# Optimization experiments

Measured on AMD Instinct MI355X. Metric: run time of the kernel, lower is better.

Reference implementation:

```python
import jax, jax.numpy as jnp
import numpy as np

# Fano-plane triples defining octonion multiplication: e_a e_b = e_c (cyclic)
_TRIPLES = [(1, 2, 4), (2, 3, 5), (3, 4, 6), (4, 5, 7), (5, 6, 1), (6, 7, 2), (7, 1, 3)]


def _oct_structure():
    """S3[i,j,k] = sign s.t. e_i * e_j = s * e_k (zero otherwise)."""
    idx = np.zeros((8, 8), dtype=np.int32)
    sgn = np.zeros((8, 8), dtype=np.float32)
    for j in range(8):
        idx[0, j] = j; sgn[0, j] = 1.0
    for i in range(1, 8):
        idx[i, 0] = i; sgn[i, 0] = 1.0
        idx[i, i] = 0; sgn[i, i] = -1.0
    for a, b, c in _TRIPLES:
        for (p, q, r) in ((a, b, c), (b, c, a), (c, a, b)):
            idx[p, q] = r; sgn[p, q] = 1.0
            idx[q, p] = r; sgn[q, p] = -1.0
    S3 = np.zeros((8, 8, 8), dtype=np.float32)
    for i in range(8):
        for j in range(8):
            S3[i, j, idx[i, j]] = sgn[i, j]
    return jnp.asarray(S3)


def _oct_full(W, S3):
    """Fold octonion structure into a dense block matrix.

    W: [8, out8, in8] per-component weights. Effective map:
      y_k = sum_{i,j} S3[i,j,k] * W_i @ x_j  ->  M[k*out8:, j*in8:] = sum_i S3[i,j,k] W_i
    Returns [8*out8, 8*in8].
    """
    M = jnp.einsum('ijk,ion->kojn', S3, W)  # [8, out8, 8, in8]
    k8, o8, j8, n8 = M.shape
    return M.reshape(k8 * o8, j8 * n8)


def setup_inputs() -> dict:
    key = jax.random.key(0)
    ks = jax.random.split(key, 6)
    B, T, D = 8, 1024, 1024
    S = 2048  # d_state = n_embd * expand_factor
    x = jax.random.normal(ks[0], (B, T, D), dtype=jnp.float32)
    h_prev = jnp.zeros((B, S), dtype=jnp.float32)
    WA = jax.random.normal(ks[1], (8, S // 8, S // 8), dtype=jnp.float32) * float(1.0 / np.sqrt(S))
    WB = jax.random.normal(ks[2], (8, S // 8, D // 8), dtype=jnp.float32) * float(1.0 / np.sqrt(D))
    WC = jax.random.normal(ks[3], (8, D // 8, S // 8), dtype=jnp.float32) * float(1.0 / np.sqrt(S))
    Wdelta = jax.random.normal(ks[4], (S, D), dtype=jnp.float32) * float(1.0 / np.sqrt(D))
    delta_bias = jnp.full((S,), -2.0, dtype=jnp.float32)
    return dict(x=x, h_prev=h_prev, WA=WA, WB=WB, WC=WC, Wdelta=Wdelta, delta_bias=delta_bias)


def reference(x, h_prev, WA, WB, WC, Wdelta, delta_bias):
    S3 = _oct_structure()
    Af = _oct_full(WA, S3)  # [S, S]
    Bf = _oct_full(WB, S3)  # [S, D]
    Cf = _oct_full(WC, S3)  # [D, S]
    # Selective gate: sigmoid(x @ Wdelta^T + bias)  [B, T, S]
    delta = jax.nn.sigmoid(jnp.einsum('btd,sd->bts', x, Wdelta) + delta_bias)
    # Input injection precomputed for all timesteps (B is time-invariant)
    Bx = jnp.einsum('btd,sd->bts', x, Bf)  # [B, T, S]

    def step(h, inp):
        bx_t, d_t = inp  # [B, S], [B, S]
        h_new = (1.0 - d_t) * h + d_t * (h @ Af.T + bx_t)
        return h_new, h_new

    h_last, hs = jax.lax.scan(step, h_prev, (jnp.swapaxes(Bx, 0, 1), jnp.swapaxes(delta, 0, 1)))
    # Readout applied to the full state history at once: y[t] = C(h[t])
    y = jnp.einsum('tbs,ds->btd', hs, Cf)  # [B, T, D]
    return y, h_last
```

## Files before the change

### kernel.cpp

```cpp
#include <hip/hip_runtime.h>
#include <hip/hip_bf16.h>

#define T_STEPS 1024
#define OFF_AFT   0ull
#define OFF_GCAT  4194304ull
#define OFF_CFT   8388608ull
#define OFF_DELTA 10485760ull
#define OFF_BX    27262976ull
#define OFF_HS    44040192ull
#define OFF_HBUF  60817408ull
#define OFF_CNT   60850176ull

typedef short short8 __attribute__((ext_vector_type(8)));
typedef float f32x4 __attribute__((ext_vector_type(4)));

__device__ __forceinline__ void build_oct_tables(int tid, int (*Is)[8], float (*Sg)[8]) {
  if (tid < 64) {
    int i = tid >> 3, j = tid & 7;
    int k = 0; float s = 0.f;
    if (i == 0)      { k = j; s = 1.f; }
    else if (j == 0) { k = i; s = 1.f; }
    else if (i == j) { k = 0; s = -1.f; }
    else {
      const int T7[7][3] = {{1,2,4},{2,3,5},{3,4,6},{4,5,7},{5,6,1},{6,7,2},{7,1,3}};
      for (int t = 0; t < 7; ++t) {
        int a = T7[t][0], b = T7[t][1], c = T7[t][2];
        const int P[3][3] = {{a,b,c},{b,c,a},{c,a,b}};
        for (int r = 0; r < 3; ++r) {
          if (i == P[r][0] && j == P[r][1]) { k = P[r][2]; s = 1.f; }
          if (i == P[r][1] && j == P[r][0]) { k = P[r][2]; s = -1.f; }
        }
      }
    }
    Is[j][k] = i; Sg[j][k] = s;
  }
  __syncthreads();
}

__device__ __forceinline__ unsigned short bf16r(float x) {
  unsigned u = __float_as_uint(x);
  return (unsigned short)((u + 0x7FFFu + ((u >> 16) & 1u)) >> 16);
}

__global__ __launch_bounds__(256) void fold_Ab(const float* __restrict__ WA, unsigned short* __restrict__ AfB) {
  __shared__ int Is[8][8]; __shared__ float Sg[8][8];
  build_oct_tables(threadIdx.x, Is, Sg);
  int g8 = blockIdx.x * 256 + threadIdx.x;
  int sp = g8 >> 8;
  int s0 = (g8 & 255) * 8;
  int k8 = sp >> 8, o = sp & 255;
  int j8 = s0 >> 8, n = s0 & 255;
  int i = Is[j8][k8]; float sg = Sg[j8][k8];
  const float* src = WA + (size_t)i * 65536 + (size_t)o * 256 + n;
  float4 f0 = *(const float4*)(src);
  float4 f1 = *(const float4*)(src + 4);
  unsigned short v[8];
  v[0] = bf16r(sg * f0.x); v[1] = bf16r(sg * f0.y); v[2] = bf16r(sg * f0.z); v[3] = bf16r(sg * f0.w);
  v[4] = bf16r(sg * f1.x); v[5] = bf16r(sg * f1.y); v[6] = bf16r(sg * f1.z); v[7] = bf16r(sg * f1.w);
  *(short8*)(AfB + (size_t)g8 * 8) = *(short8*)v;
}

__global__ __launch_bounds__(256) void fold_GC(const float* __restrict__ Wd, const float* __restrict__ WB,
                                               float* __restrict__ Gcat) {
  __shared__ int Is[8][8]; __shared__ float Sg[8][8];
  build_oct_tables(threadIdx.x, Is, Sg);
  int g4 = blockIdx.x * 256 + threadIdx.x;
  int col = (g4 & 1023) * 4;
  int d = g4 >> 10;
  float4 v;
  if (col < 2048) {
    v.x = Wd[(size_t)(col + 0) * 1024 + d];
    v.y = Wd[(size_t)(col + 1) * 1024 + d];
    v.z = Wd[(size_t)(col + 2) * 1024 + d];
    v.w = Wd[(size_t)(col + 3) * 1024 + d];
  } else {
    int sp = col - 2048;
    int k = sp >> 8;
    int j = d >> 7, n = d & 127;
    int i = Is[j][k]; float sg = Sg[j][k];
    const float* wb = WB + (size_t)i * 32768 + n;
    v.x = sg * wb[(size_t)((sp + 0) & 255) * 128];
    v.y = sg * wb[(size_t)((sp + 1) & 255) * 128];
    v.z = sg * wb[(size_t)((sp + 2) & 255) * 128];
    v.w = sg * wb[(size_t)((sp + 3) & 255) * 128];
  }
  *(float4*)(Gcat + (size_t)g4 * 4) = v;
}

__global__ __launch_bounds__(256) void fold_C(const float* __restrict__ WC, float* __restrict__ CfT) {
  __shared__ int Is[8][8]; __shared__ float Sg[8][8];
  build_oct_tables(threadIdx.x, Is, Sg);
  int g4 = blockIdx.x * 256 + threadIdx.x;
  int d0 = (g4 & 255) * 4;
  int s  = g4 >> 8;
  int j = s >> 8, n = s & 255;
  int k = d0 >> 7;
  int i = Is[j][k]; float sg = Sg[j][k];
  const float* wc = WC + (size_t)i * 32768 + n;
  float4 v;
  v.x = sg * wc[(size_t)((d0 + 0) & 127) * 256];
  v.y = sg * wc[(size_t)((d0 + 1) & 127) * 256];
  v.z = sg * wc[(size_t)((d0 + 2) & 127) * 256];
  v.w = sg * wc[(size_t)((d0 + 3) & 127) * 256];
  *(float4*)(CfT + (size_t)g4 * 4) = v;
}

__global__ __launch_bounds__(256) void init_h(const float* __restrict__ h_prev, unsigned long long* __restrict__ hx,
                                              int* __restrict__ cnt) {
  int gid = blockIdx.x * 256 + threadIdx.x;
  if (gid < 8192) {
    int c = gid >> 6, within = gid & 63;
    int pr = within >> 3, b = within & 7;
    int s = c * 16 + pr * 2;
    unsigned pk = (unsigned)bf16r(h_prev[(size_t)b * 2048 + s])
                | ((unsigned)bf16r(h_prev[(size_t)b * 2048 + s + 1]) << 16);
    hx[gid] = ((unsigned long long)pk << 32) | 0ull;
  } else {
    hx[gid] = 0x00000000FFFFFFFFull;
  }
  if (gid < 16) cnt[gid] = 0;
}

__global__ __launch_bounds__(512) void scan_dbx(const unsigned short* __restrict__ AfB,
                                                float* __restrict__ dlt, float* __restrict__ Bx,
                                                float* __restrict__ hs,
                                                unsigned long long* __restrict__ hx,
                                                const float* __restrict__ h_prev, float* __restrict__ hlast,
                                                const float* __restrict__ X, const float* __restrict__ G,
                                                const float* __restrict__ bias, int* __restrict__ chunkCnt) {
  __shared__ __attribute__((aligned(16))) unsigned short Sm[4 * 128 * 40];
  const int bid = blockIdx.x;
  const int tid = threadIdx.x;
  const int lane = tid & 63;

  if (bid >= 128) {
    const int gi = bid - 128;
    const int bn = gi & 31;
    const int bmSeq = gi >> 5;
    const int ck = bmSeq >> 3, bb = bmSeq & 7;
    const int bm = ck + 8 * bb;
    unsigned short* Ah = Sm;
    unsigned short* Al = Ah + 128 * 40;
    unsigned short* Bh = Al + 128 * 40;
    unsigned short* Bl = Bh + 128 * 40;
    const int w8 = tid >> 6;
    const int wr = w8 >> 2, wc = w8 & 3;
    const int lr = lane & 15, lk = lane >> 4;

    f32x4 acc[4][2];
    #pragma unroll
    for (int a = 0; a < 4; ++a) { acc[a][0] = (f32x4){0.f,0.f,0.f,0.f}; acc[a][1] = (f32x4){0.f,0.f,0.f,0.f}; }

    for (int kt = 0; kt < 1024; kt += 32) {
      {
        int row = tid >> 2, kq = tid & 3;
        const float* ar = X + (size_t)(bm * 128 + row) * 1024 + kt + kq * 8;
        float4 f0 = *(const float4*)(ar);
        float4 f1 = *(const float4*)(ar + 4);
        float vv[8] = {f0.x, f0.y, f0.z, f0.w, f1.x, f1.y, f1.z, f1.w};
        unsigned* ah32 = (unsigned*)Ah + row * 20 + kq * 4;
        unsigned* al32 = (unsigned*)Al + row * 20 + kq * 4;
        #pragma unroll
        for (int j = 0; j < 4; ++j) {
          unsigned short h0 = bf16r(vv[2 * j]), h1 = bf16r(vv[2 * j + 1]);
          float r0 = vv[2 * j]     - __uint_as_float((unsigned)h0 << 16);
          float r1 = vv[2 * j + 1] - __uint_as_float((unsigned)h1 << 16);
          ah32[j] = (unsigned)h0 | ((unsigned)h1 << 16);
          al32[j] = (unsigned)bf16r(r0) | ((unsigned)bf16r(r1) << 16);
        }
      }
      {
        int kr = tid >> 4, cg = tid & 15;
        const float* br = G + (size_t)(kt + kr) * 4096 + bn * 128 + cg * 8;
        float4 f0 = *(const float4*)(br);
        float4 f1 = *(const float4*)(br + 4);
        float vv[8] = {f0.x, f0.y, f0.z, f0.w, f1.x, f1.y, f1.z, f1.w};
        #pragma unroll
        for (int e = 0; e < 8; ++e) {
          int n = cg * 8 + e;
          unsigned short h = bf16r(vv[e]);
          float r = vv[e] - __uint_as_float((unsigned)h << 16);
          Bh[n * 40 + kr] = h;
          Bl[n * 40 + kr] = bf16r(r);
        }
      }
      __syncthreads();
      short8 ahf[4], alf[4], bhf[2], blf[2];
      #pragma unroll
      for (int f = 0; f < 4; ++f) {
        int ma = (wr * 64 + f * 16 + lr) * 40 + lk * 8;
        ahf[f] = *(const short8*)(Ah + ma);
        alf[f] = *(const short8*)(Al + ma);
      }
      #pragma unroll
      for (int e = 0; e < 2; ++e) {
        int nb2 = (wc * 32 + e * 16 + lr) * 40 + lk * 8;
        bhf[e] = *(const short8*)(Bh + nb2);
        blf[e] = *(const short8*)(Bl + nb2);
      }
      #pragma unroll
      for (int fm = 0; fm < 4; ++fm)
        #pragma unroll
        for (int fn = 0; fn < 2; ++fn) {
          acc[fm][fn] = __builtin_amdgcn_mfma_f32_16x16x32_bf16(ahf[fm], bhf[fn], acc[fm][fn], 0, 0, 0);
          acc[fm][fn] = __builtin_amdgcn_mfma_f32_16x16x32_bf16(ahf[fm], blf[fn], acc[fm][fn], 0, 0, 0);
          acc[fm][fn] = __builtin_amdgcn_mfma_f32_16x16x32_bf16(alf[fm], bhf[fn], acc[fm][fn], 0, 0, 0);
        }
      __syncthreads();
    }
    const bool isDelta = (bn < 16);
    #pragma unroll
    for (int fm = 0; fm < 4; ++fm) {
      #pragma unroll
      for (int rr = 0; rr < 4; ++rr) {
        int r = bm * 128 + wr * 64 + fm * 16 + lk * 4 + rr;
        int t = r & 1023, b = r >> 10;
        size_t base = ((size_t)t * 8 + b) * 2048;
        #pragma unroll
        for (int fn = 0; fn < 2; ++fn) {
          int n = bn * 128 + wc * 32 + fn * 16 + lr;
          float v = acc[fm][fn][rr];
          if (isDelta) {
            v += bias[n];
            v = 1.0f / (1.0f + expf(-v));
            __hip_atomic_store(&dlt[base + n], v, __ATOMIC_RELAXED, __HIP_MEMORY_SCOPE_SYSTEM);
          } else {
            __hip_atomic_store(&Bx[base + (n - 2048)], v, __ATOMIC_RELAXED, __HIP_MEMORY_SCOPE_SYSTEM);
          }
        }
      }
    }
    __syncthreads();
    if (tid == 0)
      __hip_atomic_fetch_add(&chunkCnt[ck], 1, __ATOMIC_RELAXED, __HIP_MEMORY_SCOPE_SYSTEM);
    return;
  }

  float* red = (float*)Sm;
  const int wg = bid;
  const int w = tid >> 6;
  const int row = lane & 15;
  const int g4 = lane >> 4;
  const int nb = lane & 7;

  short8 afr[8];
  {
    const unsigned short* ab = AfB + (size_t)(wg * 16 + row) * 2048 + w * 256 + g4 * 8;
    #pragma unroll
    for (int q = 0; q < 8; ++q)
      afr[q] = *(const short8*)(ab + q * 32);
  }
  const int S0 = (g4 & 1) * 32 + nb;

  const int ub = tid >> 3, usp = (tid & 7) * 2;
  const int pword = wg * 64 + (tid & 7) * 8 + ub;
  float hr0 = 0.f, hr1 = 0.f;
  if (tid < 64) {
    hr0 = h_prev[(size_t)ub * 2048 + wg * 16 + usp];
    hr1 = h_prev[(size_t)ub * 2048 + wg * 16 + usp + 1];
  }

  #pragma unroll 1
  for (int t = 0; t < T_STEPS; ++t) {
    float2 dv = make_float2(0.f, 0.f), bxv = make_float2(0.f, 0.f);
    if (tid < 64) {
      if ((t & 127) == 0) {
        const int ck = t >> 7;
        while (__hip_atomic_load(&chunkCnt[ck], __ATOMIC_RELAXED, __HIP_MEMORY_SCOPE_SYSTEM) < 256)
          __builtin_amdgcn_s_sleep(16);
      }
      size_t off = ((size_t)t * 8 + ub) * 2048 + wg * 16 + usp;
      dv  = *(const float2*)(dlt + off);
      bxv = *(const float2*)(Bx + off);
    }
    const unsigned want = (unsigned)t;
    const unsigned long long* bq = hx + (size_t)(t & 1) * 8192 + (size_t)w * 1024 + lane;
    unsigned long long wv[16];
    #pragma unroll
    for (int p = 0; p < 16; ++p)
      wv[p] = __hip_atomic_load(bq + p * 64, __ATOMIC_RELAXED, __HIP_MEMORY_SCOPE_SYSTEM);
    int fails = 0;
    for (;;) {
      bool stale = false;
      #pragma unroll
      for (int p = 0; p < 16; ++p) stale |= ((unsigned)wv[p] != want);
      if (!__any(stale)) break;
      if (++fails > 4) __builtin_amdgcn_s_sleep(1);
      #pragma unroll
      for (int p = 0; p < 16; ++p)
        if ((unsigned)wv[p] != want)
          wv[p] = __hip_atomic_load(bq + p * 64, __ATOMIC_RELAXED, __HIP_MEMORY_SCOPE_SYSTEM);
    }
    unsigned hi[16];
    #pragma unroll
    for (int p = 0; p < 16; ++p) hi[p] = (unsigned)(wv[p] >> 32);

    f32x4 acc = {0.f, 0.f, 0.f, 0.f};
    #pragma unroll
    for (int q = 0; q < 8; ++q) {
      union { unsigned d[4]; short8 v; } bb;
      #pragma unroll
      for (int u = 0; u < 4; ++u) {
        int S = S0 + u * 8;
        unsigned c0 = __shfl(hi[2 * q],     S, 64);
        unsigned c1 = __shfl(hi[2 * q + 1], S, 64);
        bb.d[u] = (g4 & 2) ? c1 : c0;
      }
      acc = __builtin_amdgcn_mfma_f32_16x16x32_bf16(afr[q], bb.v, acc, 0, 0, 0);
    }
    if (row < 8) {
      #pragma unroll
      for (int r = 0; r < 4; ++r)
        red[w * 144 + (g4 * 4 + r) * 9 + row] = acc[r];
    }
    __syncthreads();
    if (tid < 64) {
      __builtin_amdgcn_s_setprio(1);
      float o0 = 0.f, o1 = 0.f;
      #pragma unroll
      for (int ww = 0; ww < 8; ++ww) {
        o0 += red[ww * 144 + usp * 9 + ub];
        o1 += red[ww * 144 + (usp + 1) * 9 + ub];
      }
      float h0 = fmaf(dv.x, o0 + bxv.x - hr0, hr0);
      float h1 = fmaf(dv.y, o1 + bxv.y - hr1, hr1);
      hr0 = h0; hr1 = h1;
      unsigned pk = (unsigned)bf16r(h0) | ((unsigned)bf16r(h1) << 16);
      unsigned long long wval = ((unsigned long long)pk << 32) | (unsigned long long)(unsigned)(t + 1);
      __hip_atomic_store(hx + (size_t)((t + 1) & 1) * 8192 + pword, wval,
                         __ATOMIC_RELAXED, __HIP_MEMORY_SCOPE_SYSTEM);
      __builtin_amdgcn_s_setprio(0);
      size_t off = ((size_t)t * 8 + ub) * 2048 + wg * 16 + usp;
      *(float2*)(hs + off) = make_float2(h0, h1);
      if (t == T_STEPS - 1)
        *(float2*)(hlast + (size_t)ub * 2048 + wg * 16 + usp) = make_float2(h0, h1);
    }
    __syncthreads();
  }
}

__global__ __launch_bounds__(256) void gemm_y(const float* __restrict__ HS, const float* __restrict__ CfT,
                                              float* __restrict__ out) {
  __shared__ unsigned short As[128 * 40];
  __shared__ unsigned short Bs[128 * 40];
  const int bn = blockIdx.x, bm = blockIdx.y;
  const int tid = threadIdx.x;
  const int lane = tid & 63;
  const int w = tid >> 6;
  const int wr = w >> 1, wc = w & 1;
  const int lr = lane & 15, lk = lane >> 4;

  f32x4 acc[4][4];
  #pragma unroll
  for (int a = 0; a < 4; ++a)
    #pragma unroll
    for (int b = 0; b < 4; ++b) acc[a][b] = (f32x4){0.f, 0.f, 0.f, 0.f};

  for (int kt = 0; kt < 2048; kt += 32) {
    {
      int row = tid >> 1, kh = tid & 1;
      int rg = bm * 128 + row;
      const float* ar = HS + (size_t)((rg & 1023) * 8 + (rg >> 10)) * 2048 + kt + kh * 16;
      float vv[16];
      #pragma unroll
      for (int q = 0; q < 4; ++q) {
        float4 f = *(const float4*)(ar + q * 4);
        vv[q * 4 + 0] = f.x; vv[q * 4 + 1] = f.y; vv[q * 4 + 2] = f.z; vv[q * 4 + 3] = f.w;
      }
      unsigned* a32 = (unsigned*)As + row * 20 + kh * 8;
      #pragma unroll
      for (int j = 0; j < 8; ++j)
        a32[j] = (unsigned)bf16r(vv[2 * j]) | ((unsigned)bf16r(vv[2 * j + 1]) << 16);
    }
    {
      int kr = tid >> 3, cg = tid & 7;
      const float* br = CfT + (size_t)(kt + kr) * 1024 + bn * 128 + cg * 16;
      #pragma unroll
      for (int q = 0; q < 4; ++q) {
        float4 f = *(const float4*)(br + q * 4);
        float vv[4] = {f.x, f.y, f.z, f.w};
        #pragma unroll
        for (int e = 0; e < 4; ++e)
          Bs[(cg * 16 + q * 4 + e) * 40 + kr] = bf16r(vv[e]);
      }
    }
    __syncthreads();
    short8 aF[4], bF[4];
    #pragma unroll
    for (int f = 0; f < 4; ++f) {
      aF[f] = *(const short8*)(As + (wr * 64 + f * 16 + lr) * 40 + lk * 8);
      bF[f] = *(const short8*)(Bs + (wc * 64 + f * 16 + lr) * 40 + lk * 8);
    }
    #pragma unroll
    for (int fm = 0; fm < 4; ++fm)
      #pragma unroll
      for (int fn = 0; fn < 4; ++fn)
        acc[fm][fn] = __builtin_amdgcn_mfma_f32_16x16x32_bf16(aF[fm], bF[fn], acc[fm][fn], 0, 0, 0);
    __syncthreads();
  }
  #pragma unroll
  for (int fm = 0; fm < 4; ++fm)
    #pragma unroll
    for (int rr = 0; rr < 4; ++rr) {
      size_t rg = bm * 128 + wr * 64 + fm * 16 + lk * 4 + rr;
      #pragma unroll
      for (int fn = 0; fn < 4; ++fn) {
        int n = bn * 128 + wc * 64 + fn * 16 + lr;
        out[rg * 1024 + n] = acc[fm][fn][rr];
      }
    }
}

extern "C" void kernel_launch(void* const* d_in, const int* in_sizes, int n_in,
                              void* d_out, int out_size, void* d_ws, size_t ws_size,
                              hipStream_t stream) {
  const float* x      = (const float*)d_in[0];
  const float* h_prev = (const float*)d_in[1];
  const float* WA     = (const float*)d_in[2];
  const float* WB     = (const float*)d_in[3];
  const float* WC     = (const float*)d_in[4];
  const float* Wd     = (const float*)d_in[5];
  const float* bias   = (const float*)d_in[6];
  float* out = (float*)d_out;
  float* w = (float*)d_ws;
  unsigned short* AfB = (unsigned short*)(w + OFF_AFT);
  float* Gcat = w + OFF_GCAT;
  float* CfT  = w + OFF_CFT;
  float* dlt  = w + OFF_DELTA;
  float* Bx   = w + OFF_BX;
  float* hs   = w + OFF_HS;
  unsigned long long* hx = (unsigned long long*)(w + OFF_HBUF);
  int* chunkCnt = (int*)(w + OFF_CNT);

  fold_Ab<<<2048, 256, 0, stream>>>(WA, AfB);
  fold_GC<<<4096, 256, 0, stream>>>(Wd, WB, Gcat);
  fold_C <<<2048, 256, 0, stream>>>(WC, CfT);
  init_h <<<64,   256, 0, stream>>>(h_prev, hx, chunkCnt);
  scan_dbx<<<2176, 512, 0, stream>>>(AfB, dlt, Bx, hs, hx, h_prev, out + 8388608,
                                     x, Gcat, bias, chunkCnt);
  gemm_y<<<dim3(8, 64), 256, 0, stream>>>(hs, CfT, out);
}
```

Baseline: 3.704 ms.

## Fuse readout GEMM into scan kernel, overlapping it with the recurrence per chunk

Drops the separate gemm_y launch and adds 512 extra blocks to the persistent scan kernel. Each new block waits on a per-128-timestep progress counter, then computes its 128x128 readout tile from the finished hidden states. This lets the readout run on otherwise idle CUs while the sequential scan continues. The scan now double-buffers its reduction scratch, writes hs with atomic stores and bumps the counter after a vmcnt wait. The risks are spin-waiting blocks taking CU slots the scan blocks need (a deadlock if the scheduler runs them first) and extra memory-ordering overhead in the latency-critical scan loop.

```diff
diff --git a/kernel.cpp b/kernel.cpp
--- a/kernel.cpp
+++ b/kernel.cpp
@@ -118,20 +118,95 @@
   } else {
     hx[gid] = 0x00000000FFFFFFFFull;
   }
-  if (gid < 16) cnt[gid] = 0;
-}
-
-__global__ __launch_bounds__(512) void scan_dbx(const unsigned short* __restrict__ AfB,
-                                                float* __restrict__ dlt, float* __restrict__ Bx,
-                                                float* __restrict__ hs,
-                                                unsigned long long* __restrict__ hx,
-                                                const float* __restrict__ h_prev, float* __restrict__ hlast,
-                                                const float* __restrict__ X, const float* __restrict__ G,
-                                                const float* __restrict__ bias, int* __restrict__ chunkCnt) {
+  if (gid < 32) cnt[gid] = 0;
+}
+
+__global__ __launch_bounds__(512) void scan_dbx_y(const unsigned short* __restrict__ AfB,
+                                                  float* __restrict__ dlt, float* __restrict__ Bx,
+                                                  float* __restrict__ hs,
+                                                  unsigned long long* __restrict__ hx,
+                                                  const float* __restrict__ h_prev, float* __restrict__ hlast,
+                                                  const float* __restrict__ X, const float* __restrict__ G,
+                                                  const float* __restrict__ bias,
+                                                  const float* __restrict__ CfT, float* __restrict__ out,
+                                                  int* __restrict__ chunkCnt, int* __restrict__ scanProg) {
   __shared__ __attribute__((aligned(16))) unsigned short Sm[4 * 128 * 40];
   const int bid = blockIdx.x;
   const int tid = threadIdx.x;
   const int lane = tid & 63;
+
+  if (bid >= 2176) {
+    const int gi = bid - 2176;
+    const int ck = gi >> 6;
+    const int idx = gi & 63;
+    const int bm = (idx >> 3) * 8 + ck;
+    const int bn = idx & 7;
+    if (tid == 0) {
+      while (__hip_atomic_load(&scanProg[ck], __ATOMIC_RELAXED, __HIP_MEMORY_SCOPE_SYSTEM) < 128)
+        __builtin_amdgcn_s_sleep(32);
+    }
+    __syncthreads();
+    unsigned short* As = Sm;
+    unsigned short* Bs = Sm + 128 * 40;
+    const int w8 = tid >> 6;
+    const int wr = w8 >> 2, wc = w8 & 3;
+    const int lr = lane & 15, lk = lane >> 4;
+
+    f32x4 acc[4][2];
+    #pragma unroll
+    for (int a = 0; a < 4; ++a) { acc[a][0] = (f32x4){0.f,0.f,0.f,0.f}; acc[a][1] = (f32x4){0.f,0.f,0.f,0.f}; }
+
+    for (int kt = 0; kt < 2048; kt += 32) {
+      {
+        int row = tid >> 2, kq = tid & 3;
+        int rg = bm * 128 + row;
+        const float* ar = hs + (size_t)((rg & 1023) * 8 + (rg >> 10)) * 2048 + kt + kq * 8;
+        float4 f0 = *(const float4*)(ar);
+        float4 f1 = *(const float4*)(ar + 4);
+        float vv[8] = {f0.x, f0.y, f0.z, f0.w, f1.x, f1.y, f1.z, f1.w};
+        unsigned* a32 = (unsigned*)As + row * 20 + kq * 4;
+        #pragma unroll
+        for (int j = 0; j < 4; ++j)
+          a32[j] = (unsigned)bf16r(vv[2 * j]) | ((unsigned)bf16r(vv[2 * j + 1]) << 16);
+      }
+      {
+        int kr = tid >> 4, cg = tid & 15;
+        const float* br = CfT + (size_t)(kt + kr) * 1024 + bn * 128 + cg * 8;
+        float4 f0 = *(const float4*)(br);
+        float4 f1 = *(const float4*)(br + 4);
+        float vv[8] = {f0.x, f0.y, f0.z, f0.w, f1.x, f1.y, f1.z, f1.w};
+        #pragma unroll
+        for (int e = 0; e < 8; ++e)
+          Bs[(cg * 8 + e) * 40 + kr] = bf16r(vv[e]);
+      }
+      __syncthreads();
+      short8 aF[4], bF[2];
+      #pragma unroll
+      for (int f = 0; f < 4; ++f)
+        aF[f] = *(const short8*)(As + (wr * 64 + f * 16 + lr) * 40 + lk * 8);
+      #pragma unroll
+      for (int e = 0; e < 2; ++e)
+        bF[e] = *(const short8*)(Bs + (wc * 32 + e * 16 + lr) * 40 + lk * 8);
+      #pragma unroll
+      for (int fm = 0; fm < 4; ++fm)
+        #pragma unroll
+        for (int fn = 0; fn < 2; ++fn)
+          acc[fm][fn] = __builtin_amdgcn_mfma_f32_16x16x32_bf16(aF[fm], bF[fn], acc[fm][fn], 0, 0, 0);
+      __syncthreads();
+    }
+    #pragma unroll
+    for (int fm = 0; fm < 4; ++fm)
+      #pragma unroll
+      for (int rr = 0; rr < 4; ++rr) {
+        size_t rg = bm * 128 + wr * 64 + fm * 16 + lk * 4 + rr;
+        #pragma unroll
+        for (int fn = 0; fn < 2; ++fn) {
+          int n = bn * 128 + wc * 32 + fn * 16 + lr;
+          out[rg * 1024 + n] = acc[fm][fn][rr];
+        }
+      }
+    return;
+  }
 
   if (bid >= 128) {
     const int gi = bid - 128;
@@ -308,10 +383,11 @@
       }
       acc = __builtin_amdgcn_mfma_f32_16x16x32_bf16(afr[q], bb.v, acc, 0, 0, 0);
     }
+    float* rb = &red[(t & 1) * 1152];
     if (row < 8) {
       #pragma unroll
       for (int r = 0; r < 4; ++r)
-        red[w * 144 + (g4 * 4 + r) * 9 + row] = acc[r];
+        rb[w * 144 + (g4 * 4 + r) * 9 + row] = acc[r];
     }
     __syncthreads();
     if (tid < 64) {
@@ -319,8 +395,8 @@
       float o0 = 0.f, o1 = 0.f;
       #pragma unroll
       for (int ww = 0; ww < 8; ++ww) {
-        o0 += red[ww * 144 + usp * 9 + ub];
-        o1 += red[ww * 144 + (usp + 1) * 9 + ub];
+        o0 += rb[ww * 144 + usp * 9 + ub];
+        o1 += rb[ww * 144 + (usp + 1) * 9 + ub];
       }
       float h0 = fmaf(dv.x, o0 + bxv.x - hr0, hr0);
       float h1 = fmaf(dv.y, o1 + bxv.y - hr1, hr1);
@@ -331,84 +407,18 @@
                          __ATOMIC_RELAXED, __HIP_MEMORY_SCOPE_SYSTEM);
       __builtin_amdgcn_s_setprio(0);
       size_t off = ((size_t)t * 8 + ub) * 2048 + wg * 16 + usp;
-      *(float2*)(hs + off) = make_float2(h0, h1);
+      union { float2 f; unsigned long long u; } hsv; hsv.f = make_float2(h0, h1);
+      __hip_atomic_store((unsigned long long*)(hs + off), hsv.u,
+                         __ATOMIC_RELAXED, __HIP_MEMORY_SCOPE_SYSTEM);
       if (t == T_STEPS - 1)
         *(float2*)(hlast + (size_t)ub * 2048 + wg * 16 + usp) = make_float2(h0, h1);
-    }
-    __syncthreads();
-  }
-}
-
-__global__ __launch_bounds__(256) void gemm_y(const float* __restrict__ HS, const float* __restrict__ CfT,
-                                              float* __restrict__ out) {
-  __shared__ unsigned short As[128 * 40];
-  __shared__ unsigned short Bs[128 * 40];
-  const int bn = blockIdx.x, bm = blockIdx.y;
-  const int tid = threadIdx.x;
-  const int lane = tid & 63;
-  const int w = tid >> 6;
-  const int wr = w >> 1, wc = w & 1;
-  const int lr = lane & 15, lk = lane >> 4;
-
-  f32x4 acc[4][4];
-  #pragma unroll
-  for (int a = 0; a < 4; ++a)
-    #pragma unroll
-    for (int b = 0; b < 4; ++b) acc[a][b] = (f32x4){0.f, 0.f, 0.f, 0.f};
-
-  for (int kt = 0; kt < 2048; kt += 32) {
-    {
-      int row = tid >> 1, kh = tid & 1;
-      int rg = bm * 128 + row;
-      const float* ar = HS + (size_t)((rg & 1023) * 8 + (rg >> 10)) * 2048 + kt + kh * 16;
-      float vv[16];
-      #pragma unroll
-      for (int q = 0; q < 4; ++q) {
-        float4 f = *(const float4*)(ar + q * 4);
-        vv[q * 4 + 0] = f.x; vv[q * 4 + 1] = f.y; vv[q * 4 + 2] = f.z; vv[q * 4 + 3] = f.w;
-      }
-      unsigned* a32 = (unsigned*)As + row * 20 + kh * 8;
-      #pragma unroll
-      for (int j = 0; j < 8; ++j)
-        a32[j] = (unsigned)bf16r(vv[2 * j]) | ((unsigned)bf16r(vv[2 * j + 1]) << 16);
-    }
-    {
-      int kr = tid >> 3, cg = tid & 7;
-      const float* br = CfT + (size_t)(kt + kr) * 1024 + bn * 128 + cg * 16;
-      #pragma unroll
-      for (int q = 0; q < 4; ++q) {
-        float4 f = *(const float4*)(br + q * 4);
-        float vv[4] = {f.x, f.y, f.z, f.w};
-        #pragma unroll
-        for (int e = 0; e < 4; ++e)
-          Bs[(cg * 16 + q * 4 + e) * 40 + kr] = bf16r(vv[e]);
-      }
-    }
-    __syncthreads();
-    short8 aF[4], bF[4];
-    #pragma unroll
-    for (int f = 0; f < 4; ++f) {
-      aF[f] = *(const short8*)(As + (wr * 64 + f * 16 + lr) * 40 + lk * 8);
-      bF[f] = *(const short8*)(Bs + (wc * 64 + f * 16 + lr) * 40 + lk * 8);
-    }
-    #pragma unroll
-    for (int fm = 0; fm < 4; ++fm)
-      #pragma unroll
-      for (int fn = 0; fn < 4; ++fn)
-        acc[fm][fn] = __builtin_amdgcn_mfma_f32_16x16x32_bf16(aF[fm], bF[fn], acc[fm][fn], 0, 0, 0);
-    __syncthreads();
-  }
-  #pragma unroll
-  for (int fm = 0; fm < 4; ++fm)
-    #pragma unroll
-    for (int rr = 0; rr < 4; ++rr) {
-      size_t rg = bm * 128 + wr * 64 + fm * 16 + lk * 4 + rr;
-      #pragma unroll
-      for (int fn = 0; fn < 4; ++fn) {
-        int n = bn * 128 + wc * 64 + fn * 16 + lr;
-        out[rg * 1024 + n] = acc[fm][fn][rr];
-      }
-    }
+      if ((t & 127) == 127) {
+        asm volatile("s_waitcnt vmcnt(0)" ::: "memory");
+        if (tid == 0)
+          __hip_atomic_fetch_add(&scanProg[t >> 7], 1, __ATOMIC_RELAXED, __HIP_MEMORY_SCOPE_SYSTEM);
+      }
+    }
+  }
 }
 
 extern "C" void kernel_launch(void* const* d_in, const int* in_sizes, int n_in,
@@ -431,12 +441,12 @@
   float* hs   = w + OFF_HS;
   unsigned long long* hx = (unsigned long long*)(w + OFF_HBUF);
   int* chunkCnt = (int*)(w + OFF_CNT);
+  int* scanProg = chunkCnt + 16;
 
   fold_Ab<<<2048, 256, 0, stream>>>(WA, AfB);
   fold_GC<<<4096, 256, 0, stream>>>(Wd, WB, Gcat);
   fold_C <<<2048, 256, 0, stream>>>(WC, CfT);
   init_h <<<64,   256, 0, stream>>>(h_prev, hx, chunkCnt);
-  scan_dbx<<<2176, 512, 0, stream>>>(AfB, dlt, Bx, hs, hx, h_prev, out + 8388608,
-                                     x, Gcat, bias, chunkCnt);
-  gemm_y<<<dim3(8, 64), 256, 0, stream>>>(hs, CfT, out);
-}
+  scan_dbx_y<<<2688, 512, 0, stream>>>(AfB, dlt, Bx, hs, hx, h_prev, out + 8388608,
+                                       x, Gcat, bias, CfT, out, chunkCnt, scanProg);
+}
```

Result: slower. 4.184 ms (+13.0%).
